# Kernel tuning notes

Hardware: AMD Instinct MI355X
Metric: run time of the kernel (lower is better)

## Reference

```python
import jax, jax.numpy as jnp
import numpy as np

N_NODES = 50000
N_EDGES = 800000
IN_SIZE, HID_SIZE, OUT_SIZE = 512, 128, 64


def _graph_conv(feat, src, dst, W, b, out_norm, in_norm, activation=None):
    # DGL GraphConv with norm='both': h' = D_in^{-1/2} A D_out^{-1/2} (X W) + b
    x = feat * out_norm[:, None]          # scale by source (out-degree) norm
    x = x @ W                             # dense transform first (in >= out)
    msg = x[src]                          # gather per-edge messages [E, d]
    agg = jax.ops.segment_sum(msg, dst, num_segments=N_NODES)
    h = agg * in_norm[:, None] + b
    if activation is not None:
        h = activation(h)
    return h


def setup_inputs() -> dict:
    key = jax.random.key(0)
    k1, k2, k3, k4, k5, k6, k7 = jax.random.split(key, 7)
    features = jax.random.normal(k1, (N_NODES, IN_SIZE), dtype=jnp.float32)
    src = jax.random.randint(k2, (N_EDGES,), 0, N_NODES, dtype=jnp.int64)
    dst = jax.random.randint(k3, (N_EDGES,), 0, N_NODES, dtype=jnp.int64)
    # Glorot-style init as in dglnn.GraphConv
    W1 = jax.random.normal(k4, (IN_SIZE, HID_SIZE), dtype=jnp.float32) * (1.0 / np.sqrt(IN_SIZE))
    b1 = jnp.zeros((HID_SIZE,), dtype=jnp.float32)
    W2 = jax.random.normal(k5, (HID_SIZE, OUT_SIZE), dtype=jnp.float32) * (1.0 / np.sqrt(HID_SIZE))
    b2 = jnp.zeros((OUT_SIZE,), dtype=jnp.float32)
    return {"features": features, "W1": W1, "b1": b1, "W2": W2, "b2": b2,
            "src": src, "dst": dst}


def reference(features, W1, b1, W2, b2, src, dst):
    ones = jnp.ones((N_EDGES,), dtype=features.dtype)
    out_deg = jax.ops.segment_sum(ones, src, num_segments=N_NODES)
    in_deg = jax.ops.segment_sum(ones, dst, num_segments=N_NODES)
    out_norm = jax.lax.rsqrt(jnp.clip(out_deg, 1.0))  # deg clamped to >=1 as in DGL
    in_norm = jax.lax.rsqrt(jnp.clip(in_deg, 1.0))
    h = _graph_conv(features, src, dst, W1, b1, out_norm, in_norm, activation=jax.nn.relu)
    # dropout omitted (eval mode)
    h = _graph_conv(h, src, dst, W2, b2, out_norm, in_norm, activation=None)
    return h
```

## Files before the change

kernel.cpp:

```cpp
#include <hip/hip_runtime.h>

#define N_NODES 50000
#define IN_SIZE 512
#define HID 128
#define OUT 64
#define NB 256
#define SHIFT 7
#define NBUCK 391
#define NBINS8 12500

typedef _Float16 f16x8 __attribute__((ext_vector_type(8)));
typedef _Float16 f16x4 __attribute__((ext_vector_type(4)));
typedef float    f32x4 __attribute__((ext_vector_type(4)));

__device__ __forceinline__ bool detect_w(const int* p, int t, int* sh) {
    if (t < 64) {
        unsigned long long m = __ballot(p[2 * t + 1] == 0);
        if (t == 0) *sh = (m == ~0ull) ? 1 : 0;
    }
    __syncthreads();
    return *sh != 0;
}

__device__ __forceinline__ int load_idx(const void* p, int e, bool w) {
    return w ? (int)((const long long*)p)[e] : ((const int*)p)[e];
}

__global__ __launch_bounds__(256) void k_hist_wt(const void* __restrict__ srcp,
                                                 const void* __restrict__ dstp,
                                                 int* __restrict__ hist,
                                                 unsigned int* __restrict__ spart,
                                                 int E, int EPB,
                                                 const float* __restrict__ W1, _Float16* __restrict__ W1T,
                                                 const float* __restrict__ W2, _Float16* __restrict__ W2T) {
    const int t = threadIdx.x, b = blockIdx.x;
    if (b >= NB) {
        int i = (b - NB) * 256 + t;
        if (i < IN_SIZE * HID) {
            int k = i >> 7, n = i & (HID - 1);
            W1T[(size_t)n * IN_SIZE + k] = (_Float16)W1[i];
        } else {
            int j = i - IN_SIZE * HID;
            if (j < HID * OUT) {
                int k = j >> 6, n = j & (OUT - 1);
                W2T[(size_t)n * HID + k] = (_Float16)W2[j];
            }
        }
        return;
    }
    __shared__ unsigned int sbins[NBINS8];
    __shared__ int dbins[NBUCK];
    __shared__ int shw;
    for (int i = t; i < NBINS8; i += 256) sbins[i] = 0;
    for (int i = t; i < NBUCK; i += 256) dbins[i] = 0;
    bool w = detect_w((const int*)dstp, t, &shw);
    __syncthreads();
    int eend = min(E, (b + 1) * EPB);
    for (int e = b * EPB + t; e < eend; e += 256) {
        int s = load_idx(srcp, e, w);
        int d = load_idx(dstp, e, w);
        atomicAdd(&dbins[d >> SHIFT], 1);
        atomicAdd(&sbins[s >> 2], 1u << ((s & 3) << 3));
    }
    __syncthreads();
    for (int i = t; i < NBUCK; i += 256) hist[i * NB + b] = dbins[i];
    for (int i = t; i < NBINS8; i += 256) spart[(size_t)b * NBINS8 + i] = sbins[i];
}

__global__ __launch_bounds__(256) void k_scanA(int* __restrict__ hist, int* __restrict__ bsum) {
    __shared__ int s[256];
    const int t = threadIdx.x, g = blockIdx.x;
    int v = hist[g * NB + t];
    s[t] = v;
    __syncthreads();
    for (int off = 1; off < 256; off <<= 1) {
        int u = (t >= off) ? s[t - off] : 0;
        __syncthreads();
        s[t] += u;
        __syncthreads();
    }
    hist[g * NB + t] = s[t] - v;
    if (t == 255) bsum[g] = s[255];
}

__global__ __launch_bounds__(512) void k_scanB(const int* __restrict__ bsum, int* __restrict__ bb) {
    __shared__ int s[512];
    const int t = threadIdx.x;
    int v = (t < NBUCK) ? bsum[t] : 0;
    s[t] = v;
    __syncthreads();
    for (int off = 1; off < 512; off <<= 1) {
        int u = (t >= off) ? s[t - off] : 0;
        __syncthreads();
        s[t] += u;
        __syncthreads();
    }
    if (t <= NBUCK) bb[t] = s[t] - v;
}

__global__ __launch_bounds__(256) void k_cscatter(const void* __restrict__ srcp,
                                                  const void* __restrict__ dstp,
                                                  const int* __restrict__ hist,
                                                  const int* __restrict__ bb,
                                                  unsigned int* __restrict__ tmp,
                                                  int E, int EPB) {
    __shared__ int cur[NBUCK];
    __shared__ int shw;
    const int t = threadIdx.x, b = blockIdx.x;
    for (int i = t; i < NBUCK; i += 256) cur[i] = hist[i * NB + b] + bb[i];
    bool w = detect_w((const int*)dstp, t, &shw);
    __syncthreads();
    int eend = min(E, (b + 1) * EPB);
    for (int e = b * EPB + t; e < eend; e += 256) {
        int s = load_idx(srcp, e, w);
        int d = load_idx(dstp, e, w);
        int pos = atomicAdd(&cur[d >> SHIFT], 1);
        tmp[pos] = (unsigned int)s | ((unsigned int)(d & 127) << 16);
    }
}

__global__ __launch_bounds__(256) void k_fine(const unsigned int* __restrict__ tmp,
                                              const int* __restrict__ bb,
                                              const unsigned int* __restrict__ partial,
                                              int* __restrict__ rp,
                                              int* __restrict__ esrc,
                                              float* __restrict__ innorm,
                                              float* __restrict__ onorm) {
    __shared__ int fcnt[128];
    __shared__ int sc[128];
    __shared__ int fcur[128];
    __shared__ int rs[256][4];
    const int t = threadIdx.x, u = blockIdx.x;
    const int e0 = bb[u], e1 = bb[u + 1];
    if (t < 128) fcnt[t] = 0;
    __syncthreads();
    for (int e = e0 + t; e < e1; e += 256)
        atomicAdd(&fcnt[tmp[e] >> 16], 1);
    {
        const int wrd = t & 31, grp = t >> 5;
        const int wd = u * 32 + wrd;
        int c0 = 0, c1 = 0, c2 = 0, c3 = 0;
        if (wd < NBINS8) {
            for (int b = grp * 32; b < grp * 32 + 32; ++b) {
                unsigned int v = partial[(size_t)b * NBINS8 + wd];
                c0 += (int)(v & 255u);
                c1 += (int)((v >> 8) & 255u);
                c2 += (int)((v >> 16) & 255u);
                c3 += (int)(v >> 24);
            }
        }
        rs[t][0] = c0; rs[t][1] = c1; rs[t][2] = c2; rs[t][3] = c3;
    }
    __syncthreads();
    if (t < 32) {
        const int wd = u * 32 + t;
        if (wd < NBINS8) {
            int d0 = 0, d1 = 0, d2 = 0, d3 = 0;
            for (int g = 0; g < 8; ++g) {
                d0 += rs[g * 32 + t][0]; d1 += rs[g * 32 + t][1];
                d2 += rs[g * 32 + t][2]; d3 += rs[g * 32 + t][3];
            }
            if (d0 < 1) d0 = 1; if (d1 < 1) d1 = 1;
            if (d2 < 1) d2 = 1; if (d3 < 1) d3 = 1;
            int n0 = 4 * wd;
            if (n0     < N_NODES) onorm[n0]     = 1.0f / sqrtf((float)d0);
            if (n0 + 1 < N_NODES) onorm[n0 + 1] = 1.0f / sqrtf((float)d1);
            if (n0 + 2 < N_NODES) onorm[n0 + 2] = 1.0f / sqrtf((float)d2);
            if (n0 + 3 < N_NODES) onorm[n0 + 3] = 1.0f / sqrtf((float)d3);
        }
    }
    if (t < 128) sc[t] = fcnt[t];
    __syncthreads();
    for (int off = 1; off < 128; off <<= 1) {
        int v = (t < 128 && t >= off) ? sc[t - off] : 0;
        __syncthreads();
        if (t < 128) sc[t] += v;
        __syncthreads();
    }
    if (t < 128) {
        int base = e0 + sc[t] - fcnt[t];
        fcur[t] = base;
        int node = u * 128 + t;
        if (node < N_NODES) {
            rp[node] = base;
            int c = fcnt[t]; if (c < 1) c = 1;
            innorm[node] = 1.0f / sqrtf((float)c);
        }
    }
    if (u == NBUCK - 1 && t == 0) rp[N_NODES] = e1;
    __syncthreads();
    for (int e = e0 + t; e < e1; e += 256) {
        unsigned int p = tmp[e];
        int pos = atomicAdd(&fcur[p >> 16], 1);
        esrc[pos] = (int)(p & 0xFFFFu);
    }
}

__global__ __launch_bounds__(256) void k_gemm1_mfma(const float* __restrict__ A,
                                                    const _Float16* __restrict__ BT,
                                                    const float* __restrict__ onorm,
                                                    _Float16* __restrict__ X) {
    const int tid  = threadIdx.x;
    const int wave = tid >> 6, lane = tid & 63;
    const int lm = lane & 15, lq = lane >> 4;
    const int row0 = blockIdx.x * 64;

    int arow = row0 + wave * 16 + lm;
    if (arow >= N_NODES) arow = N_NODES - 1;
    const float* aptr = A + (size_t)arow * IN_SIZE + lq * 8;
    const _Float16* bptr = BT + (size_t)lm * IN_SIZE + lq * 8;

    f32x4 acc[8];
#pragma unroll
    for (int nt = 0; nt < 8; ++nt) acc[nt] = (f32x4){0.f, 0.f, 0.f, 0.f};

#pragma unroll 2
    for (int k0 = 0; k0 < IN_SIZE; k0 += 32) {
        float4 a0 = *(const float4*)(aptr + k0);
        float4 a1 = *(const float4*)(aptr + k0 + 4);
        f16x8 af = {(_Float16)a0.x, (_Float16)a0.y, (_Float16)a0.z, (_Float16)a0.w,
                    (_Float16)a1.x, (_Float16)a1.y, (_Float16)a1.z, (_Float16)a1.w};
#pragma unroll
        for (int nt = 0; nt < 8; ++nt) {
            f16x8 bf = *(const f16x8*)(bptr + (size_t)nt * 16 * IN_SIZE + k0);
            acc[nt] = __builtin_amdgcn_mfma_f32_16x16x32_f16(af, bf, acc[nt], 0, 0, 0);
        }
    }
#pragma unroll
    for (int i = 0; i < 4; ++i) {
        int row = row0 + wave * 16 + lq * 4 + i;
        if (row < N_NODES) {
            float on = onorm[row];
            _Float16* o = X + (size_t)row * HID + lm;
#pragma unroll
            for (int nt = 0; nt < 8; ++nt)
                o[nt * 16] = (_Float16)(acc[nt][i] * on);
        }
    }
}

#define LDH 136
__global__ __launch_bounds__(256) void k_agg1_fused(const _Float16* __restrict__ X, const int* __restrict__ rp,
                                                    const int* __restrict__ esrc, const float* __restrict__ innorm,
                                                    const float* __restrict__ onorm, const float* __restrict__ b1,
                                                    const _Float16* __restrict__ W2T, _Float16* __restrict__ X2) {
    __shared__ _Float16 Hs[16 * LDH];
    const int t = threadIdx.x;
    const int ln = t >> 4;
    const int c  = (t & 15) << 3;
    const int n  = blockIdx.x * 16 + ln;
    const int e0 = rp[n], e1 = rp[n + 1];
    float a[8] = {0.f, 0.f, 0.f, 0.f, 0.f, 0.f, 0.f, 0.f};
    int e = e0;
    for (; e + 3 < e1; e += 4) {
        int s0 = esrc[e], s1 = esrc[e + 1], s2 = esrc[e + 2], s3 = esrc[e + 3];
        f16x8 v0 = *(const f16x8*)&X[(size_t)s0 * HID + c];
        f16x8 v1 = *(const f16x8*)&X[(size_t)s1 * HID + c];
        f16x8 v2 = *(const f16x8*)&X[(size_t)s2 * HID + c];
        f16x8 v3 = *(const f16x8*)&X[(size_t)s3 * HID + c];
#pragma unroll
        for (int j = 0; j < 8; ++j)
            a[j] += ((float)v0[j] + (float)v1[j]) + ((float)v2[j] + (float)v3[j]);
    }
    for (; e < e1; ++e) {
        f16x8 v = *(const f16x8*)&X[(size_t)esrc[e] * HID + c];
#pragma unroll
        for (int j = 0; j < 8; ++j) a[j] += (float)v[j];
    }
    const float inn = innorm[n], on = onorm[n];
    float4 bA = *(const float4*)&b1[c];
    float4 bB = *(const float4*)&b1[c + 4];
    const float bv[8] = {bA.x, bA.y, bA.z, bA.w, bB.x, bB.y, bB.z, bB.w};
    f16x8 h;
#pragma unroll
    for (int j = 0; j < 8; ++j)
        h[j] = (_Float16)(fmaxf(a[j] * inn + bv[j], 0.f) * on);
    *(f16x8*)&Hs[ln * LDH + c] = h;
    __syncthreads();

    const int wave = t >> 6, lane = t & 63;
    const int lm = lane & 15, lq = lane >> 4;
    f32x4 acc = (f32x4){0.f, 0.f, 0.f, 0.f};
#pragma unroll
    for (int k0 = 0; k0 < HID; k0 += 32) {
        f16x8 af = *(const f16x8*)&Hs[lm * LDH + k0 + lq * 8];
        f16x8 bf = *(const f16x8*)&W2T[(size_t)(wave * 16 + lm) * HID + k0 + lq * 8];
        acc = __builtin_amdgcn_mfma_f32_16x16x32_f16(af, bf, acc, 0, 0, 0);
    }
    const int n0 = blockIdx.x * 16;
#pragma unroll
    for (int i = 0; i < 4; ++i) {
        int row = n0 + lq * 4 + i;
        X2[(size_t)row * OUT + wave * 16 + lm] = (_Float16)acc[i];
    }
}

__global__ __launch_bounds__(256) void k_agg2(const _Float16* __restrict__ X2, const int* __restrict__ rp,
                                              const int* __restrict__ esrc, const float* __restrict__ innorm,
                                              const float* __restrict__ b2, float* __restrict__ out) {
    const int n = blockIdx.x * 32 + (threadIdx.x >> 3);
    const int c = (threadIdx.x & 7) << 3;
    if (n >= N_NODES) return;
    const int e0 = rp[n], e1 = rp[n + 1];
    float a[8] = {0.f, 0.f, 0.f, 0.f, 0.f, 0.f, 0.f, 0.f};
    int e = e0;
    for (; e + 3 < e1; e += 4) {
        int s0 = esrc[e], s1 = esrc[e + 1], s2 = esrc[e + 2], s3 = esrc[e + 3];
        f16x8 v0 = *(const f16x8*)&X2[(size_t)s0 * OUT + c];
        f16x8 v1 = *(const f16x8*)&X2[(size_t)s1 * OUT + c];
        f16x8 v2 = *(const f16x8*)&X2[(size_t)s2 * OUT + c];
        f16x8 v3 = *(const f16x8*)&X2[(size_t)s3 * OUT + c];
#pragma unroll
        for (int j = 0; j < 8; ++j)
            a[j] += ((float)v0[j] + (float)v1[j]) + ((float)v2[j] + (float)v3[j]);
    }
    for (; e < e1; ++e) {
        f16x8 v = *(const f16x8*)&X2[(size_t)esrc[e] * OUT + c];
#pragma unroll
        for (int j = 0; j < 8; ++j) a[j] += (float)v[j];
    }
    const float inn = innorm[n];
    float4 bA = *(const float4*)&b2[c];
    float4 bB = *(const float4*)&b2[c + 4];
    float* o = out + (size_t)n * OUT + c;
    *(float4*)o       = make_float4(a[0] * inn + bA.x, a[1] * inn + bA.y,
                                    a[2] * inn + bA.z, a[3] * inn + bA.w);
    *(float4*)(o + 4) = make_float4(a[4] * inn + bB.x, a[5] * inn + bB.y,
                                    a[6] * inn + bB.z, a[7] * inn + bB.w);
}

extern "C" void kernel_launch(void* const* d_in, const int* in_sizes, int n_in,
                              void* d_out, int out_size, void* d_ws, size_t ws_size,
                              hipStream_t stream) {
    const float* feat = (const float*)d_in[0];
    const float* W1   = (const float*)d_in[1];
    const float* b1   = (const float*)d_in[2];
    const float* W2   = (const float*)d_in[3];
    const float* b2   = (const float*)d_in[4];
    const void*  srcp = (const void*)d_in[5];
    const void*  dstp = (const void*)d_in[6];
    const int    E    = in_sizes[5];
    float* out = (float*)d_out;

    char* w = (char*)d_ws;
    size_t off = 0;
    auto alloc = [&](size_t bytes) -> void* {
        off = (off + 255) & ~(size_t)255;
        void* p = w + off;
        off += bytes;
        return p;
    };
    int*   hist    = (int*)alloc((size_t)NBUCK * NB * 4);
    int*   bsum    = (int*)alloc((size_t)NBUCK * 4);
    int*   bb      = (int*)alloc((size_t)(NBUCK + 1) * 4);
    int*   rp      = (int*)alloc((size_t)(N_NODES + 1) * 4);
    unsigned int* spart = (unsigned int*)alloc((size_t)NB * NBINS8 * 4);
    unsigned int* tmp   = (unsigned int*)alloc((size_t)E * 4);
    int*   esrc    = (int*)alloc((size_t)E * 4);
    float* onorm   = (float*)alloc((size_t)N_NODES * 4);
    float* innorm  = (float*)alloc((size_t)N_NODES * 4);
    _Float16* W1T  = (_Float16*)alloc((size_t)IN_SIZE * HID * 2);
    _Float16* W2T  = (_Float16*)alloc((size_t)HID * OUT * 2);
    _Float16* X1   = (_Float16*)alloc((size_t)N_NODES * HID * 2);
    _Float16* X2   = (_Float16*)alloc((size_t)N_NODES * OUT * 2);
    (void)ws_size; (void)n_in; (void)out_size;

    const int EPB = (E + NB - 1) / NB;
    const int WTB = (IN_SIZE * HID + HID * OUT + 255) / 256;

    k_hist_wt<<<NB + WTB, 256, 0, stream>>>(srcp, dstp, hist, spart, E, EPB, W1, W1T, W2, W2T);
    k_scanA<<<NBUCK, 256, 0, stream>>>(hist, bsum);
    k_scanB<<<1, 512, 0, stream>>>(bsum, bb);
    k_cscatter<<<NB, 256, 0, stream>>>(srcp, dstp, hist, bb, tmp, E, EPB);
    k_fine<<<NBUCK, 256, 0, stream>>>(tmp, bb, spart, rp, esrc, innorm, onorm);

    k_gemm1_mfma<<<(N_NODES + 63) / 64, 256, 0, stream>>>(feat, W1T, onorm, X1);
    k_agg1_fused<<<(N_NODES + 15) / 16, 256, 0, stream>>>(X1, rp, esrc, innorm, onorm, b1, W2T, X2);
    k_agg2<<<(N_NODES + 31) / 32, 256, 0, stream>>>(X2, rp, esrc, innorm, b2, out);
}
```

Baseline: 313.0 us.

## Stage W1 in LDS and run GEMM1 as persistent waves with A prefetch

GEMM1 now copies the full fp16 W1 transpose into padded shared memory once per block. It launches 256 persistent blocks of 8 waves that grid-stride over 16-row tiles, and software-prefetches A three k-steps ahead. This is meant to cut repeated global/L2 reads of B and hide the latency of the streaming fp32 A loads. In exchange it uses about 130KB of LDS per block, which limits occupancy to one block per CU. The row bound check was dropped, which is safe only because N_NODES divides evenly by 16.

```diff
diff --git a/kernel.cpp b/kernel.cpp
--- a/kernel.cpp
+++ b/kernel.cpp
@@ -196,40 +196,54 @@
     }
 }
 
-__global__ __launch_bounds__(256) void k_gemm1_mfma(const float* __restrict__ A,
+#define LDB 520
+__global__ __launch_bounds__(512) void k_gemm1_mfma(const float* __restrict__ A,
                                                     const _Float16* __restrict__ BT,
                                                     const float* __restrict__ onorm,
                                                     _Float16* __restrict__ X) {
-    const int tid  = threadIdx.x;
-    const int wave = tid >> 6, lane = tid & 63;
+    __shared__ _Float16 Bs[128 * LDB];
+    const int t = threadIdx.x;
+    const int wave = t >> 6, lane = t & 63;
     const int lm = lane & 15, lq = lane >> 4;
-    const int row0 = blockIdx.x * 64;
-
-    int arow = row0 + wave * 16 + lm;
-    if (arow >= N_NODES) arow = N_NODES - 1;
-    const float* aptr = A + (size_t)arow * IN_SIZE + lq * 8;
-    const _Float16* bptr = BT + (size_t)lm * IN_SIZE + lq * 8;
-
-    f32x4 acc[8];
-#pragma unroll
-    for (int nt = 0; nt < 8; ++nt) acc[nt] = (f32x4){0.f, 0.f, 0.f, 0.f};
-
-#pragma unroll 2
-    for (int k0 = 0; k0 < IN_SIZE; k0 += 32) {
-        float4 a0 = *(const float4*)(aptr + k0);
-        float4 a1 = *(const float4*)(aptr + k0 + 4);
-        f16x8 af = {(_Float16)a0.x, (_Float16)a0.y, (_Float16)a0.z, (_Float16)a0.w,
-                    (_Float16)a1.x, (_Float16)a1.y, (_Float16)a1.z, (_Float16)a1.w};
-#pragma unroll
-        for (int nt = 0; nt < 8; ++nt) {
-            f16x8 bf = *(const f16x8*)(bptr + (size_t)nt * 16 * IN_SIZE + k0);
-            acc[nt] = __builtin_amdgcn_mfma_f32_16x16x32_f16(af, bf, acc[nt], 0, 0, 0);
-        }
-    }
-#pragma unroll
-    for (int i = 0; i < 4; ++i) {
-        int row = row0 + wave * 16 + lq * 4 + i;
-        if (row < N_NODES) {
+
+    for (int i = t; i < 128 * 64; i += 512) {
+        int r = i >> 6, c = (i & 63) << 3;
+        *(f16x8*)&Bs[r * LDB + c] = *(const f16x8*)(BT + ((size_t)r << 9) + c);
+    }
+    __syncthreads();
+
+    const int slot = blockIdx.x * 8 + wave;
+    for (int g = slot; g < N_NODES / 16; g += 2048) {
+        const float* aptr = A + ((size_t)(g * 16 + lm) << 9) + lq * 8;
+        f32x4 acc[8];
+#pragma unroll
+        for (int nt = 0; nt < 8; ++nt) acc[nt] = (f32x4){0.f, 0.f, 0.f, 0.f};
+
+        float4 pa[3][2];
+#pragma unroll
+        for (int p = 0; p < 3; ++p) {
+            pa[p][0] = *(const float4*)(aptr + p * 32);
+            pa[p][1] = *(const float4*)(aptr + p * 32 + 4);
+        }
+#pragma unroll
+        for (int kt = 0; kt < 16; ++kt) {
+            float4 a0 = pa[kt % 3][0];
+            float4 a1 = pa[kt % 3][1];
+            if (kt + 3 < 16) {
+                pa[kt % 3][0] = *(const float4*)(aptr + (kt + 3) * 32);
+                pa[kt % 3][1] = *(const float4*)(aptr + (kt + 3) * 32 + 4);
+            }
+            f16x8 af = {(_Float16)a0.x, (_Float16)a0.y, (_Float16)a0.z, (_Float16)a0.w,
+                        (_Float16)a1.x, (_Float16)a1.y, (_Float16)a1.z, (_Float16)a1.w};
+#pragma unroll
+            for (int nt = 0; nt < 8; ++nt) {
+                f16x8 bf = *(const f16x8*)&Bs[(nt * 16 + lm) * LDB + kt * 32 + lq * 8];
+                acc[nt] = __builtin_amdgcn_mfma_f32_16x16x32_f16(af, bf, acc[nt], 0, 0, 0);
+            }
+        }
+#pragma unroll
+        for (int i = 0; i < 4; ++i) {
+            int row = g * 16 + lq * 4 + i;
             float on = onorm[row];
             _Float16* o = X + (size_t)row * HID + lm;
 #pragma unroll
@@ -374,7 +388,7 @@
     k_cscatter<<<NB, 256, 0, stream>>>(srcp, dstp, hist, bb, tmp, E, EPB);
     k_fine<<<NBUCK, 256, 0, stream>>>(tmp, bb, spart, rp, esrc, innorm, onorm);
 
-    k_gemm1_mfma<<<(N_NODES + 63) / 64, 256, 0, stream>>>(feat, W1T, onorm, X1);
+    k_gemm1_mfma<<<256, 512, 0, stream>>>(feat, W1T, onorm, X1);
     k_agg1_fused<<<(N_NODES + 15) / 16, 256, 0, stream>>>(X1, rp, esrc, innorm, onorm, b1, W2T, X2);
     k_agg2<<<(N_NODES + 31) / 32, 256, 0, stream>>>(X2, rp, esrc, innorm, b2, out);
 }
```

After: 382.4 us. 1.22x slower.

## Stage GEMM1 weight tiles in double-buffered LDS and prefetch A two steps ahead

Applied to the files above, without the earlier changes.

The first-layer GEMM now loads each 128x32 half-precision weight slice cooperatively into a double-buffered shared-memory tile with padding, so MFMA operands come from LDS rather than each wave re-reading the weights from global memory. A-row loads are software-prefetched two K-steps ahead in registers to hide global latency. The cost is a block barrier per K-step, extra register pressure from the prefetch buffers, and about 22 KB of LDS per block, which may reduce occupancy.

```diff
diff --git a/kernel.cpp b/kernel.cpp
--- a/kernel.cpp
+++ b/kernel.cpp
@@ -196,10 +196,12 @@
     }
 }
 
+#define LDA 44
 __global__ __launch_bounds__(256) void k_gemm1_mfma(const float* __restrict__ A,
                                                     const _Float16* __restrict__ BT,
                                                     const float* __restrict__ onorm,
                                                     _Float16* __restrict__ X) {
+    __shared__ _Float16 Bs[2][128 * LDA];
     const int tid  = threadIdx.x;
     const int wave = tid >> 6, lane = tid & 63;
     const int lm = lane & 15, lq = lane >> 4;
@@ -208,22 +210,56 @@
     int arow = row0 + wave * 16 + lm;
     if (arow >= N_NODES) arow = N_NODES - 1;
     const float* aptr = A + (size_t)arow * IN_SIZE + lq * 8;
-    const _Float16* bptr = BT + (size_t)lm * IN_SIZE + lq * 8;
+
+    const int bn = tid >> 1, bh = tid & 1;
+    const _Float16* bptr = BT + (size_t)bn * IN_SIZE + bh * 16;
 
     f32x4 acc[8];
 #pragma unroll
     for (int nt = 0; nt < 8; ++nt) acc[nt] = (f32x4){0.f, 0.f, 0.f, 0.f};
 
-#pragma unroll 2
-    for (int k0 = 0; k0 < IN_SIZE; k0 += 32) {
-        float4 a0 = *(const float4*)(aptr + k0);
-        float4 a1 = *(const float4*)(aptr + k0 + 4);
+    {
+        f16x8 b0 = *(const f16x8*)(bptr);
+        f16x8 b1 = *(const f16x8*)(bptr + 8);
+        *(f16x8*)&Bs[0][bn * LDA + bh * 16]     = b0;
+        *(f16x8*)&Bs[0][bn * LDA + bh * 16 + 8] = b1;
+    }
+    float4 pa0_0 = *(const float4*)(aptr);
+    float4 pa0_1 = *(const float4*)(aptr + 4);
+    float4 pa1_0 = *(const float4*)(aptr + 32);
+    float4 pa1_1 = *(const float4*)(aptr + 36);
+    __syncthreads();
+
+#pragma unroll
+    for (int kt = 0; kt < 16; ++kt) {
+        const int cur = kt & 1;
+        float4 a0 = (kt & 1) ? pa1_0 : pa0_0;
+        float4 a1 = (kt & 1) ? pa1_1 : pa0_1;
+        if (kt + 2 < 16) {
+            if (kt & 1) {
+                pa1_0 = *(const float4*)(aptr + (kt + 2) * 32);
+                pa1_1 = *(const float4*)(aptr + (kt + 2) * 32 + 4);
+            } else {
+                pa0_0 = *(const float4*)(aptr + (kt + 2) * 32);
+                pa0_1 = *(const float4*)(aptr + (kt + 2) * 32 + 4);
+            }
+        }
+        f16x8 nb0, nb1;
+        if (kt + 1 < 16) {
+            nb0 = *(const f16x8*)(bptr + (kt + 1) * 32);
+            nb1 = *(const f16x8*)(bptr + (kt + 1) * 32 + 8);
+        }
         f16x8 af = {(_Float16)a0.x, (_Float16)a0.y, (_Float16)a0.z, (_Float16)a0.w,
                     (_Float16)a1.x, (_Float16)a1.y, (_Float16)a1.z, (_Float16)a1.w};
 #pragma unroll
         for (int nt = 0; nt < 8; ++nt) {
-            f16x8 bf = *(const f16x8*)(bptr + (size_t)nt * 16 * IN_SIZE + k0);
+            f16x8 bf = *(const f16x8*)&Bs[cur][(nt * 16 + lm) * LDA + lq * 8];
             acc[nt] = __builtin_amdgcn_mfma_f32_16x16x32_f16(af, bf, acc[nt], 0, 0, 0);
+        }
+        if (kt + 1 < 16) {
+            *(f16x8*)&Bs[cur ^ 1][bn * LDA + bh * 16]     = nb0;
+            *(f16x8*)&Bs[cur ^ 1][bn * LDA + bh * 16 + 8] = nb1;
+            __syncthreads();
         }
     }
 #pragma unroll
```

Result: faster. 274.6 us (-12.3%).

## Stage GEMM1 tiles through LDS with async global_load_lds triple buffering

Applied to the files above, without the earlier changes.

Replaces the direct global-memory loads of A and BT in the first-layer MFMA GEMM with asynchronous global_load_lds copies into a triple-buffered, XOR-swizzled shared-memory ring. Loads for tile k+3 are issued while tile k is computed, with explicit vmcnt waits and barriers per k-step. The aim is to hide global latency and share the B tiles across waves instead of having each wave fetch them from global. In exchange it adds two block barriers per k-step and uses about 48 KB of LDS, which may lower occupancy.

```diff
diff --git a/kernel.cpp b/kernel.cpp
--- a/kernel.cpp
+++ b/kernel.cpp
@@ -196,36 +196,92 @@
     }
 }
 
+__device__ __forceinline__ void gl_lds16f(const float* g, float* l) {
+    __builtin_amdgcn_global_load_lds((const __attribute__((address_space(1))) void*)g,
+                                     (__attribute__((address_space(3))) void*)l, 16, 0, 0);
+}
+__device__ __forceinline__ void gl_lds16h(const _Float16* g, _Float16* l) {
+    __builtin_amdgcn_global_load_lds((const __attribute__((address_space(1))) void*)g,
+                                     (__attribute__((address_space(3))) void*)l, 16, 0, 0);
+}
+
 __global__ __launch_bounds__(256) void k_gemm1_mfma(const float* __restrict__ A,
                                                     const _Float16* __restrict__ BT,
                                                     const float* __restrict__ onorm,
                                                     _Float16* __restrict__ X) {
+    __shared__ float    Abuf[3 * 2048];
+    __shared__ _Float16 Bbuf[3 * 4096];
     const int tid  = threadIdx.x;
     const int wave = tid >> 6, lane = tid & 63;
     const int lm = lane & 15, lq = lane >> 4;
     const int row0 = blockIdx.x * 64;
 
-    int arow = row0 + wave * 16 + lm;
-    if (arow >= N_NODES) arow = N_NODES - 1;
-    const float* aptr = A + (size_t)arow * IN_SIZE + lq * 8;
-    const _Float16* bptr = BT + (size_t)lm * IN_SIZE + lq * 8;
+    const int raj0 = (wave * 2 + 0) * 8 + (lane >> 3);
+    const int raj1 = (wave * 2 + 1) * 8 + (lane >> 3);
+    const int acol = ((lane & 7) ^ (lane >> 3)) * 4;
+    const int arow0 = min(row0 + raj0, N_NODES - 1);
+    const int arow1 = min(row0 + raj1, N_NODES - 1);
+    const float* aS0 = A + (size_t)arow0 * IN_SIZE + acol;
+    const float* aS1 = A + (size_t)arow1 * IN_SIZE + acol;
+    const int rb0 = wave * 32 + (lane >> 2);
+    const int rb1 = wave * 32 + 16 + (lane >> 2);
+    const int bc0 = (((lane & 3) ^ ((rb0 >> 1) & 3))) * 8;
+    const int bc1 = (((lane & 3) ^ ((rb1 >> 1) & 3))) * 8;
+    const _Float16* bS0 = BT + (size_t)rb0 * IN_SIZE + bc0;
+    const _Float16* bS1 = BT + (size_t)rb1 * IN_SIZE + bc1;
+
+    float*    aD0 = Abuf + (wave * 2 + 0) * 256;
+    float*    aD1 = Abuf + (wave * 2 + 1) * 256;
+    _Float16* bD0 = Bbuf + (wave * 2 + 0) * 512;
+    _Float16* bD1 = Bbuf + (wave * 2 + 1) * 512;
+
+#define STAGE1(b, t) do {                              \
+        gl_lds16f(aS0 + (t) * 32, aD0 + (b) * 2048);   \
+        gl_lds16f(aS1 + (t) * 32, aD1 + (b) * 2048);   \
+        gl_lds16h(bS0 + (t) * 32, bD0 + (b) * 4096);   \
+        gl_lds16h(bS1 + (t) * 32, bD1 + (b) * 4096);   \
+    } while (0)
 
     f32x4 acc[8];
 #pragma unroll
     for (int nt = 0; nt < 8; ++nt) acc[nt] = (f32x4){0.f, 0.f, 0.f, 0.f};
 
-#pragma unroll 2
-    for (int k0 = 0; k0 < IN_SIZE; k0 += 32) {
-        float4 a0 = *(const float4*)(aptr + k0);
-        float4 a1 = *(const float4*)(aptr + k0 + 4);
+    STAGE1(0, 0);
+    STAGE1(1, 1);
+    STAGE1(2, 2);
+    asm volatile("s_waitcnt vmcnt(8)" ::: "memory");
+    __builtin_amdgcn_sched_barrier(0);
+    __builtin_amdgcn_s_barrier();
+
+    const int swA = lm & 7;
+    const int swB = (lm >> 1) & 3;
+    const char* abase = (const char*)Abuf + wave * 2048 + lm * 128;
+    const char* bbase = (const char*)Bbuf + lm * 64 + ((lq ^ swB) << 4);
+
+#pragma unroll
+    for (int kt = 0; kt < 16; ++kt) {
+        const int cur = kt % 3;
+        float4 a0 = *(const float4*)(abase + cur * 8192 + (((lq * 2)     ^ swA) << 4));
+        float4 a1 = *(const float4*)(abase + cur * 8192 + (((lq * 2 + 1) ^ swA) << 4));
         f16x8 af = {(_Float16)a0.x, (_Float16)a0.y, (_Float16)a0.z, (_Float16)a0.w,
                     (_Float16)a1.x, (_Float16)a1.y, (_Float16)a1.z, (_Float16)a1.w};
 #pragma unroll
         for (int nt = 0; nt < 8; ++nt) {
-            f16x8 bf = *(const f16x8*)(bptr + (size_t)nt * 16 * IN_SIZE + k0);
+            f16x8 bf = *(const f16x8*)(bbase + cur * 8192 + nt * 1024);
             acc[nt] = __builtin_amdgcn_mfma_f32_16x16x32_f16(af, bf, acc[nt], 0, 0, 0);
         }
-    }
+        if (kt < 15) {
+            __builtin_amdgcn_s_barrier();
+            if (kt + 3 < 16) STAGE1((kt + 3) % 3, kt + 3);
+            if (kt <= 12)      asm volatile("s_waitcnt vmcnt(8)" ::: "memory");
+            else if (kt == 13) asm volatile("s_waitcnt vmcnt(4)" ::: "memory");
+            else               asm volatile("s_waitcnt vmcnt(0)" ::: "memory");
+            __builtin_amdgcn_sched_barrier(0);
+            __builtin_amdgcn_s_barrier();
+        }
+    }
+#undef STAGE1
+
 #pragma unroll
     for (int i = 0; i < 4; ++i) {
         int row = row0 + wave * 16 + lq * 4 + i;
```

After: 274.6 us. 1.14x faster.
